# Optimization experiments

Measured on AMD Instinct MI355X. Metric: run time of the kernel, lower is better.

Reference implementation:

```python
import jax, jax.numpy as jnp
import numpy as np

B, N_DOWN, N_UP, C_IN, C_OUT, SPIRAL, NNZ = 8, 12288, 49152, 64, 32, 9, 147456


def setup_inputs() -> dict:
    key = jax.random.key(0)
    ks = jax.random.split(key, 7)
    x = jax.random.normal(ks[0], (B, N_DOWN, C_IN), dtype=jnp.float32)
    up_rows = jax.random.randint(ks[1], (NNZ,), 0, N_UP, dtype=jnp.int32)
    up_cols = jax.random.randint(ks[2], (NNZ,), 0, N_DOWN, dtype=jnp.int32)
    up_vals = jax.random.uniform(ks[3], (NNZ,), dtype=jnp.float32)
    spiral_indices = jax.random.randint(ks[4], (N_UP, SPIRAL), 0, N_UP, dtype=jnp.int32)
    weight = jax.random.normal(ks[5], (C_OUT, SPIRAL * C_IN), dtype=jnp.float32) * 0.02
    bias = jax.random.normal(ks[6], (C_OUT,), dtype=jnp.float32) * 0.02
    return {"x": x, "up_rows": up_rows, "up_cols": up_cols, "up_vals": up_vals,
            "spiral_indices": spiral_indices, "weight": weight, "bias": bias}


def reference(x, up_rows, up_cols, up_vals, spiral_indices, weight, bias):
    # Pool: sparse upsample matmul along vertex dim (dim=1)
    # gathered: [B, nnz, C_in]
    gathered = x[:, up_cols, :] * up_vals[None, :, None]
    pooled = jax.vmap(lambda g: jax.ops.segment_sum(g, up_rows, num_segments=N_UP))(gathered)  # [B, N_up, C_in]
    # SpiralConv: gather spiral neighbors, flatten, linear
    flat_idx = spiral_indices.reshape(-1)  # [N_up*SPIRAL]
    g = pooled[:, flat_idx, :].reshape(B, N_UP, SPIRAL * C_IN)
    out = jnp.einsum('bnk,ok->bno', g, weight) + bias
    return jax.nn.relu(out)
```

## Files before the change

### kernel.cpp

```cpp
#include <hip/hip_runtime.h>
#include <hip/hip_bf16.h>

#define BB 8
#define ND 12288
#define NU 49152
#define CI 64
#define CO 32
#define SP 9
#define NNZ 147456
#define KTOT (SP * CI)
#define KPAD 584

using short8 = __attribute__((ext_vector_type(8))) short;
using f32x4  = __attribute__((ext_vector_type(4))) float;

#define OFF_WBF   ((size_t)BB * NU * CI * 2)
#define OFF_CNT   (OFF_WBF   + (size_t)CO * KTOT * 2)
#define OFF_START (OFF_CNT   + (size_t)NU * 4)
#define OFF_FILL  (OFF_START + (size_t)(NU + 1) * 4 + 4)
#define OFF_PCOL  (OFF_FILL  + (size_t)NU * 4)
#define OFF_PVAL  (OFF_PCOL  + (size_t)NNZ * 4)

static __device__ __forceinline__ unsigned short f2bf(float f) {
    __hip_bfloat16 h = __float2bfloat16(f);
    return *reinterpret_cast<unsigned short*>(&h);
}

__global__ __launch_bounds__(256) void hist_kernel(
    const int* __restrict__ rows, int* __restrict__ cnt)
{
    const int i = blockIdx.x * 256 + threadIdx.x;
    atomicAdd(&cnt[rows[i]], 1);
}

__global__ __launch_bounds__(1024) void scan_kernel(
    const int* __restrict__ cnt, int* __restrict__ start, int* __restrict__ fill)
{
    __shared__ int sums[1024];
    const int t = threadIdx.x;
    const int base = t * (NU / 1024);
    int s = 0;
#pragma unroll
    for (int i = 0; i < NU / 1024; ++i) s += cnt[base + i];
    sums[t] = s;
    __syncthreads();
    for (int off = 1; off < 1024; off <<= 1) {
        const int add = (t >= off) ? sums[t - off] : 0;
        __syncthreads();
        sums[t] += add;
        __syncthreads();
    }
    int excl = sums[t] - s;
#pragma unroll
    for (int i = 0; i < NU / 1024; ++i) {
        const int c = cnt[base + i];
        start[base + i] = excl;
        fill[base + i]  = excl;
        excl += c;
    }
    if (t == 1023) start[NU] = sums[1023];
}

__global__ __launch_bounds__(256) void perm_kernel(
    const int* __restrict__ rows, const int* __restrict__ cols,
    const float* __restrict__ vals, int* __restrict__ fill,
    int* __restrict__ pcol, float* __restrict__ pval)
{
    const int i = blockIdx.x * 256 + threadIdx.x;
    const int pos = atomicAdd(&fill[rows[i]], 1);
    pcol[pos] = cols[i];
    pval[pos] = vals[i];
}

__global__ __launch_bounds__(256) void wcvt_kernel(
    const float* __restrict__ weight, unsigned short* __restrict__ wbf)
{
    const int i = blockIdx.x * 256 + threadIdx.x;
    wbf[i] = f2bf(weight[i]);
}

__global__ __launch_bounds__(256) void pool_kernel(
    const float* __restrict__ x, const int* __restrict__ start,
    const int* __restrict__ pcol, const float* __restrict__ pval,
    unsigned short* __restrict__ pooled)
{
    const int t   = blockIdx.x * 256 + threadIdx.x;
    const int row = t >> 4;
    const int cq  = (t & 15) << 2;
    const int s = start[row], e = start[row + 1];
    float4 acc[BB];
#pragma unroll
    for (int b = 0; b < BB; ++b) acc[b] = make_float4(0.f, 0.f, 0.f, 0.f);
    for (int j = s; j < e; ++j) {
        const int col = pcol[j];
        const float v = pval[j];
#pragma unroll
        for (int b = 0; b < BB; ++b) {
            const float4 xv = *(const float4*)(x + ((size_t)(b * ND + col) * CI + cq));
            acc[b].x = fmaf(v, xv.x, acc[b].x);
            acc[b].y = fmaf(v, xv.y, acc[b].y);
            acc[b].z = fmaf(v, xv.z, acc[b].z);
            acc[b].w = fmaf(v, xv.w, acc[b].w);
        }
    }
#pragma unroll
    for (int b = 0; b < BB; ++b) {
        uint2 pk;
        pk.x = (unsigned)f2bf(acc[b].x) | ((unsigned)f2bf(acc[b].y) << 16);
        pk.y = (unsigned)f2bf(acc[b].z) | ((unsigned)f2bf(acc[b].w) << 16);
        *(uint2*)(pooled + ((size_t)row * BB + b) * CI + cq) = pk;
    }
}

__global__ __launch_bounds__(512) void conv_mfma(
    const unsigned short* __restrict__ pooled, const unsigned short* __restrict__ wbf,
    const int* __restrict__ spiral, const float* __restrict__ bias,
    float* __restrict__ out)
{
    __shared__ __align__(16) unsigned short wT[CO][KPAD];

    const int tid  = threadIdx.x;
    const int b    = tid >> 6;
    const int lane = tid & 63;
    const int r    = lane & 15;
    const int kg   = lane >> 4;
    const int n0   = blockIdx.x * 16;
    const int n    = n0 + r;

    {
        const int o = tid >> 4;
        const int c = tid & 15;
#pragma unroll
        for (int j = 0; j < 9; ++j) {
            const int idx = (j * 16 + c) * 4;
            *(uint2*)&wT[o][idx] = *(const uint2*)(wbf + (size_t)o * KTOT + idx);
        }
    }

    int g[SP];
#pragma unroll
    for (int s = 0; s < SP; ++s) g[s] = spiral[n * SP + s];

    const unsigned short* abase = pooled + (size_t)b * CI + (size_t)kg * 8;

    short8 a0l,a0h,a1l,a1h,a2l,a2h,a3l,a3h,a4l,a4h,a5l,a5h,a6l,a6h,a7l,a7h,a8l,a8h;
#define LDA(vl, vh, s) \
    vl = *(const short8*)(abase + (size_t)g[s] * (BB * CI)); \
    vh = *(const short8*)(abase + (size_t)g[s] * (BB * CI) + 32)
    LDA(a0l,a0h,0); LDA(a1l,a1h,1); LDA(a2l,a2h,2); LDA(a3l,a3h,3);
    LDA(a4l,a4h,4); LDA(a5l,a5h,5); LDA(a6l,a6h,6); LDA(a7l,a7h,7);
    LDA(a8l,a8h,8);
#undef LDA
    __builtin_amdgcn_sched_barrier(0);

    __syncthreads();

    f32x4 acc0 = {0.f, 0.f, 0.f, 0.f};
    f32x4 acc1 = {0.f, 0.f, 0.f, 0.f};
    const unsigned short* w0 = &wT[r][kg * 8];
    const unsigned short* w1 = &wT[16 + r][kg * 8];

#define STEP(al, ah, s) do { \
    const short8 b00 = *(const short8*)(w0 + (s) * 64); \
    const short8 b01 = *(const short8*)(w1 + (s) * 64); \
    const short8 b10 = *(const short8*)(w0 + (s) * 64 + 32); \
    const short8 b11 = *(const short8*)(w1 + (s) * 64 + 32); \
    acc0 = __builtin_amdgcn_mfma_f32_16x16x32_bf16(al, b00, acc0, 0, 0, 0); \
    acc1 = __builtin_amdgcn_mfma_f32_16x16x32_bf16(al, b01, acc1, 0, 0, 0); \
    acc0 = __builtin_amdgcn_mfma_f32_16x16x32_bf16(ah, b10, acc0, 0, 0, 0); \
    acc1 = __builtin_amdgcn_mfma_f32_16x16x32_bf16(ah, b11, acc1, 0, 0, 0); \
  } while (0)
    STEP(a0l,a0h,0); STEP(a1l,a1h,1); STEP(a2l,a2h,2); STEP(a3l,a3h,3);
    STEP(a4l,a4h,4); STEP(a5l,a5h,5); STEP(a6l,a6h,6); STEP(a7l,a7h,7);
    STEP(a8l,a8h,8);
#undef STEP

    const float bo0 = bias[r];
    const float bo1 = bias[16 + r];
    const size_t mbase = (size_t)b * NU + n0 + kg * 4;
#pragma unroll
    for (int reg = 0; reg < 4; ++reg) {
        const size_t m = mbase + reg;
        out[m * CO + r]      = fmaxf(acc0[reg] + bo0, 0.f);
        out[m * CO + 16 + r] = fmaxf(acc1[reg] + bo1, 0.f);
    }
}

extern "C" void kernel_launch(void* const* d_in, const int* in_sizes, int n_in,
                              void* d_out, int out_size, void* d_ws, size_t ws_size,
                              hipStream_t stream) {
    const float* x      = (const float*)d_in[0];
    const int*   rows   = (const int*)d_in[1];
    const int*   cols   = (const int*)d_in[2];
    const float* vals   = (const float*)d_in[3];
    const int*   spiral = (const int*)d_in[4];
    const float* weight = (const float*)d_in[5];
    const float* bias   = (const float*)d_in[6];
    float*       out    = (float*)d_out;

    char* ws = (char*)d_ws;
    unsigned short* pooled = (unsigned short*)ws;
    unsigned short* wbf    = (unsigned short*)(ws + OFF_WBF);
    int*   cnt    = (int*)(ws + OFF_CNT);
    int*   startp = (int*)(ws + OFF_START);
    int*   fill   = (int*)(ws + OFF_FILL);
    int*   pcol   = (int*)(ws + OFF_PCOL);
    float* pval   = (float*)(ws + OFF_PVAL);

    hipMemsetAsync(cnt, 0, (size_t)NU * 4, stream);

    hist_kernel<<<NNZ / 256, 256, 0, stream>>>(rows, cnt);
    scan_kernel<<<1, 1024, 0, stream>>>(cnt, startp, fill);
    perm_kernel<<<NNZ / 256, 256, 0, stream>>>(rows, cols, vals, fill, pcol, pval);
    wcvt_kernel<<<(CO * KTOT) / 256, 256, 0, stream>>>(weight, wbf);
    pool_kernel<<<(NU * 16) / 256, 256, 0, stream>>>(x, startp, pcol, pval, pooled);

    conv_mfma<<<NU / 16, 512, 0, stream>>>(pooled, wbf, spiral, bias, out);
}
```

Before: 248.6 us.

## Use wave-shuffle scan, interleaved col/val entries, 2-way gather unroll, nontemporal output stores

The single-block scan now uses wavefront shuffles and per-thread register caching instead of a 1024-step shared-memory Hillis-Steele loop with many barriers. Column index and value are packed into one int2 per entry, so the pool kernel fetches both with one load. The pool gather loop handles two nonzeros per iteration, issuing all 16 x loads before the FMAs to expose more memory-level parallelism, at the cost of higher register pressure. Conv output stores become nontemporal to reduce cache pollution.

```diff
diff --git a/kernel.cpp b/kernel.cpp
--- a/kernel.cpp
+++ b/kernel.cpp
@@ -18,8 +18,7 @@
 #define OFF_CNT   (OFF_WBF   + (size_t)CO * KTOT * 2)
 #define OFF_START (OFF_CNT   + (size_t)NU * 4)
 #define OFF_FILL  (OFF_START + (size_t)(NU + 1) * 4 + 4)
-#define OFF_PCOL  (OFF_FILL  + (size_t)NU * 4)
-#define OFF_PVAL  (OFF_PCOL  + (size_t)NNZ * 4)
+#define OFF_PENT  (OFF_FILL  + (size_t)NU * 4)
 
 static __device__ __forceinline__ unsigned short f2bf(float f) {
     __hip_bfloat16 h = __float2bfloat16(f);
@@ -36,40 +35,53 @@
 __global__ __launch_bounds__(1024) void scan_kernel(
     const int* __restrict__ cnt, int* __restrict__ start, int* __restrict__ fill)
 {
-    __shared__ int sums[1024];
-    const int t = threadIdx.x;
-    const int base = t * (NU / 1024);
+    __shared__ int wsum[16], woff[16];
+    const int t = threadIdx.x, lane = t & 63, w = t >> 6;
+    const int base = t * 48;
+    int c[48];
     int s = 0;
 #pragma unroll
-    for (int i = 0; i < NU / 1024; ++i) s += cnt[base + i];
-    sums[t] = s;
+    for (int i = 0; i < 48; ++i) { c[i] = cnt[base + i]; s += c[i]; }
+    int incl = s;
+#pragma unroll
+    for (int d = 1; d < 64; d <<= 1) {
+        const int v = __shfl_up(incl, d, 64);
+        if (lane >= d) incl += v;
+    }
+    if (lane == 63) wsum[w] = incl;
     __syncthreads();
-    for (int off = 1; off < 1024; off <<= 1) {
-        const int add = (t >= off) ? sums[t - off] : 0;
-        __syncthreads();
-        sums[t] += add;
-        __syncthreads();
-    }
-    int excl = sums[t] - s;
-#pragma unroll
-    for (int i = 0; i < NU / 1024; ++i) {
-        const int c = cnt[base + i];
-        start[base + i] = excl;
-        fill[base + i]  = excl;
-        excl += c;
-    }
-    if (t == 1023) start[NU] = sums[1023];
+    if (w == 0 && lane < 16) {
+        const int v = wsum[lane];
+        int inc2 = v;
+#pragma unroll
+        for (int d = 1; d < 16; d <<= 1) {
+            const int u = __shfl_up(inc2, d, 16);
+            if (lane >= d) inc2 += u;
+        }
+        woff[lane] = inc2 - v;
+    }
+    __syncthreads();
+    int run = woff[w] + incl - s;
+#pragma unroll
+    for (int i = 0; i < 48; ++i) {
+        start[base + i] = run;
+        fill[base + i]  = run;
+        run += c[i];
+    }
+    if (t == 1023) start[NU] = run;
 }
 
 __global__ __launch_bounds__(256) void perm_kernel(
     const int* __restrict__ rows, const int* __restrict__ cols,
     const float* __restrict__ vals, int* __restrict__ fill,
-    int* __restrict__ pcol, float* __restrict__ pval)
+    int2* __restrict__ pent)
 {
     const int i = blockIdx.x * 256 + threadIdx.x;
     const int pos = atomicAdd(&fill[rows[i]], 1);
-    pcol[pos] = cols[i];
-    pval[pos] = vals[i];
+    int2 e;
+    e.x = cols[i];
+    e.y = __float_as_int(vals[i]);
+    pent[pos] = e;
 }
 
 __global__ __launch_bounds__(256) void wcvt_kernel(
@@ -81,8 +93,7 @@
 
 __global__ __launch_bounds__(256) void pool_kernel(
     const float* __restrict__ x, const int* __restrict__ start,
-    const int* __restrict__ pcol, const float* __restrict__ pval,
-    unsigned short* __restrict__ pooled)
+    const int2* __restrict__ pent, unsigned short* __restrict__ pooled)
 {
     const int t   = blockIdx.x * 256 + threadIdx.x;
     const int row = t >> 4;
@@ -91,16 +102,41 @@
     float4 acc[BB];
 #pragma unroll
     for (int b = 0; b < BB; ++b) acc[b] = make_float4(0.f, 0.f, 0.f, 0.f);
-    for (int j = s; j < e; ++j) {
-        const int col = pcol[j];
-        const float v = pval[j];
+
+    int j = s;
+    for (; j + 1 < e; j += 2) {
+        const int2 e0 = pent[j], e1 = pent[j + 1];
+        const float v0 = __int_as_float(e0.y), v1 = __int_as_float(e1.y);
+        float4 xv0[BB], xv1[BB];
+#pragma unroll
+        for (int b = 0; b < BB; ++b)
+            xv0[b] = *(const float4*)(x + ((size_t)(b * ND + e0.x) * CI + cq));
+#pragma unroll
+        for (int b = 0; b < BB; ++b)
+            xv1[b] = *(const float4*)(x + ((size_t)(b * ND + e1.x) * CI + cq));
+        __builtin_amdgcn_sched_barrier(0);
 #pragma unroll
         for (int b = 0; b < BB; ++b) {
-            const float4 xv = *(const float4*)(x + ((size_t)(b * ND + col) * CI + cq));
-            acc[b].x = fmaf(v, xv.x, acc[b].x);
-            acc[b].y = fmaf(v, xv.y, acc[b].y);
-            acc[b].z = fmaf(v, xv.z, acc[b].z);
-            acc[b].w = fmaf(v, xv.w, acc[b].w);
+            acc[b].x = fmaf(v0, xv0[b].x, acc[b].x);
+            acc[b].y = fmaf(v0, xv0[b].y, acc[b].y);
+            acc[b].z = fmaf(v0, xv0[b].z, acc[b].z);
+            acc[b].w = fmaf(v0, xv0[b].w, acc[b].w);
+            acc[b].x = fmaf(v1, xv1[b].x, acc[b].x);
+            acc[b].y = fmaf(v1, xv1[b].y, acc[b].y);
+            acc[b].z = fmaf(v1, xv1[b].z, acc[b].z);
+            acc[b].w = fmaf(v1, xv1[b].w, acc[b].w);
+        }
+    }
+    if (j < e) {
+        const int2 e0 = pent[j];
+        const float v0 = __int_as_float(e0.y);
+#pragma unroll
+        for (int b = 0; b < BB; ++b) {
+            const float4 xv = *(const float4*)(x + ((size_t)(b * ND + e0.x) * CI + cq));
+            acc[b].x = fmaf(v0, xv.x, acc[b].x);
+            acc[b].y = fmaf(v0, xv.y, acc[b].y);
+            acc[b].z = fmaf(v0, xv.z, acc[b].z);
+            acc[b].w = fmaf(v0, xv.w, acc[b].w);
         }
     }
 #pragma unroll
@@ -181,8 +217,8 @@
 #pragma unroll
     for (int reg = 0; reg < 4; ++reg) {
         const size_t m = mbase + reg;
-        out[m * CO + r]      = fmaxf(acc0[reg] + bo0, 0.f);
-        out[m * CO + 16 + r] = fmaxf(acc1[reg] + bo1, 0.f);
+        __builtin_nontemporal_store(fmaxf(acc0[reg] + bo0, 0.f), out + m * CO + r);
+        __builtin_nontemporal_store(fmaxf(acc1[reg] + bo1, 0.f), out + m * CO + 16 + r);
     }
 }
 
@@ -204,16 +240,15 @@
     int*   cnt    = (int*)(ws + OFF_CNT);
     int*   startp = (int*)(ws + OFF_START);
     int*   fill   = (int*)(ws + OFF_FILL);
-    int*   pcol   = (int*)(ws + OFF_PCOL);
-    float* pval   = (float*)(ws + OFF_PVAL);
+    int2*  pent   = (int2*)(ws + OFF_PENT);
 
     hipMemsetAsync(cnt, 0, (size_t)NU * 4, stream);
 
     hist_kernel<<<NNZ / 256, 256, 0, stream>>>(rows, cnt);
     scan_kernel<<<1, 1024, 0, stream>>>(cnt, startp, fill);
-    perm_kernel<<<NNZ / 256, 256, 0, stream>>>(rows, cols, vals, fill, pcol, pval);
+    perm_kernel<<<NNZ / 256, 256, 0, stream>>>(rows, cols, vals, fill, pent);
     wcvt_kernel<<<(CO * KTOT) / 256, 256, 0, stream>>>(weight, wbf);
-    pool_kernel<<<(NU * 16) / 256, 256, 0, stream>>>(x, startp, pcol, pval, pooled);
+    pool_kernel<<<(NU * 16) / 256, 256, 0, stream>>>(x, startp, pent, pooled);
 
     conv_mfma<<<NU / 16, 512, 0, stream>>>(pooled, wbf, spiral, bias, out);
 }
```

New measurement: 245.8 us. About the same (-1.1%).
